# Kernel tuning notes

Hardware: AMD Instinct MI355X
Metric: run time of the kernel (lower is better)

Reference implementation:

```python
import jax, jax.numpy as jnp
import numpy as np

FP8_MAX = 448.0  # e4m3fn max representable magnitude


def _fp8_round(t):
    # round-trip through float8_e4m3fn emulates fp8 quantization rounding
    return t.astype(jnp.float8_e4m3fn).astype(t.dtype)


def setup_inputs() -> dict:
    key = jax.random.key(0)
    kx, kw, kb, ks = jax.random.split(key, 4)
    B, S, IN, OUT = 4, 2048, 4096, 4096
    x = jax.random.normal(kx, (B, S, IN), dtype=jnp.float16)
    # build an fp8-quantized weight exactly as the torch module does
    w = jax.random.uniform(kw, (OUT, IN), dtype=jnp.float16)
    w_s = (jnp.max(jnp.abs(w)).astype(jnp.float32) / FP8_MAX).reshape(1)
    w_fp8 = ((w.astype(jnp.float32) / w_s)
             .astype(jnp.float8_e4m3fn)
             .astype(jnp.float16))
    bias = jax.random.uniform(kb, (OUT,), dtype=jnp.float16)
    input_scale = jnp.ones((1,), dtype=jnp.float32)
    return {"x": x, "weight_fp8": w_fp8, "bias": bias,
            "input_scale": input_scale, "weight_scale": w_s}


def reference(x, weight_fp8, bias, input_scale, weight_scale):
    in_s = input_scale[0]
    w_s = weight_scale[0]
    # fake-quantize input to fp8 (per-tensor scale, clamp to e4m3 range)
    xq = jnp.clip(x.astype(jnp.float32) / in_s, -FP8_MAX, FP8_MAX)
    x_dq = _fp8_round(xq) * in_s                      # [B,S,IN] f32
    # dequantize fp8 weight
    w_dq = weight_fp8.astype(jnp.float32) * w_s       # [OUT,IN] f32
    out = jnp.einsum('bsi,oi->bso', x_dq, w_dq) + bias.astype(jnp.float32)
    return out.astype(x.dtype)
```

## Files before the change

### kernel.cpp

```cpp
#include <hip/hip_runtime.h>
#include <stdint.h>

typedef float  f32x4  __attribute__((ext_vector_type(4)));
typedef float  float4v __attribute__((ext_vector_type(4)));
typedef int    i32x4  __attribute__((ext_vector_type(4)));
typedef int    i32x8  __attribute__((ext_vector_type(8)));
typedef unsigned int u32x4 __attribute__((ext_vector_type(4)));

#define BM 128
#define BN 256
#define BKB 128

__device__ __forceinline__ unsigned f32_to_e4m3_sw(float t) {
    unsigned u = __float_as_uint(t);
    unsigned s = (u >> 24) & 0x80u;
    float ax = fabsf(t);
    if (ax < 0.015625f) {
        int m = (int)rintf(ax * 512.0f);
        return s | (unsigned)m;
    }
    unsigned au = u & 0x7fffffffu;
    unsigned r = au + 0x7FFFFu + ((au >> 20) & 1u);
    return s | (((r >> 23) - 120u) << 3) | ((r >> 20) & 7u);
}

__device__ __forceinline__ unsigned pack4_e4m3(float a, float b, float c, float d) {
#if __has_builtin(__builtin_amdgcn_cvt_pk_fp8_f32)
    int v = 0;
    v = __builtin_amdgcn_cvt_pk_fp8_f32(a, b, v, false);
    v = __builtin_amdgcn_cvt_pk_fp8_f32(c, d, v, true);
    return (unsigned)v;
#else
    return f32_to_e4m3_sw(a) | (f32_to_e4m3_sw(b) << 8) |
           (f32_to_e4m3_sw(c) << 16) | (f32_to_e4m3_sw(d) << 24);
#endif
}

__global__ void quant_kernel(const float4v* __restrict__ x, u32x4* __restrict__ xout, long nx16,
                             const float4v* __restrict__ w, u32x4* __restrict__ wout, long nw16,
                             const float* __restrict__ in_scale) {
    const float inv = 1.0f / in_scale[0];
    const long stride = (long)gridDim.x * blockDim.x;
    long i0 = (long)blockIdx.x * blockDim.x + threadIdx.x;
    for (long i = i0; i < nx16; i += stride) {
        u32x4 q;
#pragma unroll
        for (int j = 0; j < 4; ++j) {
            float4v v = x[i * 4 + j];
            float t0 = fminf(fmaxf(v[0] * inv, -448.0f), 448.0f);
            float t1 = fminf(fmaxf(v[1] * inv, -448.0f), 448.0f);
            float t2 = fminf(fmaxf(v[2] * inv, -448.0f), 448.0f);
            float t3 = fminf(fmaxf(v[3] * inv, -448.0f), 448.0f);
            q[j] = pack4_e4m3(t0, t1, t2, t3);
        }
        xout[i] = q;
    }
    for (long i = i0; i < nw16; i += stride) {
        u32x4 q;
#pragma unroll
        for (int j = 0; j < 4; ++j) {
            float4v v = w[i * 4 + j];
            q[j] = pack4_e4m3(v[0], v[1], v[2], v[3]);
        }
        wout[i] = q;
    }
}


__global__ __launch_bounds__(256, 2) void gemm_kernel(
    const unsigned char* __restrict__ A,
    const unsigned char* __restrict__ W,
    const float* __restrict__ bias,
    const float* __restrict__ in_scale,
    const float* __restrict__ w_scale,
    float* __restrict__ C, int M, int N, int K)
{
    __shared__ __align__(16) unsigned char sA[BM * BKB];
    __shared__ __align__(16) unsigned char sB[BN * BKB];

    const int tid  = threadIdx.x;
    const int wave = tid >> 6;
    const int lane = tid & 63;
    const int wr   = wave >> 1;
    const int wc   = wave & 1;

    const int nwg = gridDim.x;
    int bid = blockIdx.x, wgid;
    if ((nwg & 7) == 0) { const int cpx = nwg >> 3; wgid = (bid & 7) * cpx + (bid >> 3); }
    else wgid = bid;

    const int ntn = N / BN;
    int brow, bcol;
    if (nwg % (8 * ntn) == 0) {
        const int chunkId = wgid / (8 * ntn);
        const int local   = wgid % (8 * ntn);
        brow = (chunkId * 8 + (local & 7)) * BM;
        bcol = (local >> 3) * BN;
    } else {
        brow = (wgid / ntn) * BM;
        bcol = (wgid % ntn) * BN;
    }

    const int rowInChunk = lane >> 3;
    const int pPhys      = (lane & 7) ^ rowInChunk;
    const int slotSrc    = 2 * (pPhys & 3) + (pPhys >> 2);

    f32x4 acc[4][8];
#pragma unroll
    for (int i = 0; i < 4; ++i)
#pragma unroll
        for (int j = 0; j < 8; ++j) { f32x4 z = {0.f,0.f,0.f,0.f}; acc[i][j] = z; }

    const int g = lane >> 4;

    for (int kt = 0; kt < K; kt += BKB) {
        if (kt) __syncthreads();
#pragma unroll
        for (int c = 0; c < 4; ++c) {
            const int chunk = wave * 4 + c;
            const int row   = chunk * 8 + rowInChunk;
            const unsigned char* ga = A + (long)(brow + row) * K + kt + slotSrc * 16;
            __builtin_amdgcn_global_load_lds(
                (const __attribute__((address_space(1))) unsigned int*)ga,
                (__attribute__((address_space(3))) unsigned int*)(sA + chunk * 1024), 16, 0, 0);
        }
#pragma unroll
        for (int c = 0; c < 8; ++c) {
            const int chunk = wave * 8 + c;
            const int row   = chunk * 8 + rowInChunk;
            const unsigned char* gb = W + (long)(bcol + row) * K + kt + slotSrc * 16;
            __builtin_amdgcn_global_load_lds(
                (const __attribute__((address_space(1))) unsigned int*)gb,
                (__attribute__((address_space(3))) unsigned int*)(sB + chunk * 1024), 16, 0, 0);
        }
        __syncthreads();

        i32x8 af[4];
#pragma unroll
        for (int mi = 0; mi < 4; ++mi) {
            const int row = wr * 64 + mi * 16 + (lane & 15);
            const int sl  = g ^ (row & 7);
            i32x4 lo = *(const i32x4*)(sA + row * 128 + sl * 16);
            i32x4 hi = *(const i32x4*)(sA + row * 128 + (sl ^ 4) * 16);
            i32x8 t;
            t[0]=lo[0]; t[1]=lo[1]; t[2]=lo[2]; t[3]=lo[3];
            t[4]=hi[0]; t[5]=hi[1]; t[6]=hi[2]; t[7]=hi[3];
            af[mi] = t;
        }
#pragma unroll
        for (int ni = 0; ni < 8; ++ni) {
            const int row = wc * 128 + ni * 16 + (lane & 15);
            const int sl  = g ^ (row & 7);
            i32x4 lo = *(const i32x4*)(sB + row * 128 + sl * 16);
            i32x4 hi = *(const i32x4*)(sB + row * 128 + (sl ^ 4) * 16);
            i32x8 bf;
            bf[0]=lo[0]; bf[1]=lo[1]; bf[2]=lo[2]; bf[3]=lo[3];
            bf[4]=hi[0]; bf[5]=hi[1]; bf[6]=hi[2]; bf[7]=hi[3];
#pragma unroll
            for (int mi = 0; mi < 4; ++mi)
                acc[mi][ni] = __builtin_amdgcn_mfma_scale_f32_16x16x128_f8f6f4(
                    af[mi], bf, acc[mi][ni],
                    0, 0, 0, 0x7F7F7F7F, 0, 0x7F7F7F7F);
        }
    }

    const float sc = in_scale[0] * w_scale[0];
#pragma unroll
    for (int ni = 0; ni < 8; ++ni) {
        const int n   = bcol + wc * 128 + ni * 16 + (lane & 15);
        const float bv = bias[n];
#pragma unroll
        for (int mi = 0; mi < 4; ++mi) {
            const int m0 = brow + wr * 64 + mi * 16 + ((lane >> 4) << 2);
#pragma unroll
            for (int r = 0; r < 4; ++r)
                __builtin_nontemporal_store(fmaf(acc[mi][ni][r], sc, bv),
                                            &C[(long)(m0 + r) * N + n]);
        }
    }
}

extern "C" void kernel_launch(void* const* d_in, const int* in_sizes, int n_in,
                              void* d_out, int out_size, void* d_ws, size_t ws_size,
                              hipStream_t stream) {
    const float* x    = (const float*)d_in[0];
    const float* w    = (const float*)d_in[1];
    const float* bias = (const float*)d_in[2];
    const float* in_s = (const float*)d_in[3];
    const float* w_s  = (const float*)d_in[4];
    float* out = (float*)d_out;

    const int  N   = in_sizes[2];
    const long wsz = (long)in_sizes[1];
    const int  K   = (int)(wsz / N);
    const long xsz = (long)in_sizes[0];
    const int  M   = (int)(xsz / K);

    unsigned char* xq = (unsigned char*)d_ws;
    unsigned char* wq = xq + (size_t)M * K;

    quant_kernel<<<2048, 256, 0, stream>>>((const float4v*)x, (u32x4*)xq, xsz / 16,
                                           (const float4v*)w, (u32x4*)wq, wsz / 16, in_s);

    dim3 grid((M / BM) * (N / BN));
    gemm_kernel<<<grid, 256, 0, stream>>>(xq, wq, bias, in_s, w_s, out, M, N, K);
}
```

Baseline: 164.3 us.

## Switch GEMM to single-wave 64x128 tiles without workgroup barriers

Shrinks the GEMM block tile from 128x256 with four waves to 64x128 with a single wave, so each workgroup's wave loads its whole tile and replaces __syncthreads with explicit s_waitcnt on vmcnt/lgkmcnt. The block-to-tile mapping is reworked to group blocks along rows within XCD chunks. The intent is to remove barrier overhead and raise occupancy, at the cost of less data reuse per block, more global/L2 traffic and no overlap between loads and MFMAs within a workgroup.

```diff
diff --git a/kernel.cpp b/kernel.cpp
--- a/kernel.cpp
+++ b/kernel.cpp
@@ -7,8 +7,8 @@
 typedef int    i32x8  __attribute__((ext_vector_type(8)));
 typedef unsigned int u32x4 __attribute__((ext_vector_type(4)));
 
-#define BM 128
-#define BN 256
+#define BM 64
+#define BN 128
 #define BKB 128
 
 __device__ __forceinline__ unsigned f32_to_e4m3_sw(float t) {
@@ -67,7 +67,7 @@
 }
 
 
-__global__ __launch_bounds__(256, 2) void gemm_kernel(
+__global__ __launch_bounds__(64, 2) void gemm_kernel(
     const unsigned char* __restrict__ A,
     const unsigned char* __restrict__ W,
     const float* __restrict__ bias,
@@ -78,24 +78,23 @@
     __shared__ __align__(16) unsigned char sA[BM * BKB];
     __shared__ __align__(16) unsigned char sB[BN * BKB];
 
-    const int tid  = threadIdx.x;
-    const int wave = tid >> 6;
-    const int lane = tid & 63;
-    const int wr   = wave >> 1;
-    const int wc   = wave & 1;
+    const int lane = threadIdx.x;
 
     const int nwg = gridDim.x;
     int bid = blockIdx.x, wgid;
     if ((nwg & 7) == 0) { const int cpx = nwg >> 3; wgid = (bid & 7) * cpx + (bid >> 3); }
     else wgid = bid;
 
-    const int ntn = N / BN;
+    const int nrows = M / BM;
+    const int ntn   = N / BN;
     int brow, bcol;
-    if (nwg % (8 * ntn) == 0) {
-        const int chunkId = wgid / (8 * ntn);
-        const int local   = wgid % (8 * ntn);
-        brow = (chunkId * 8 + (local & 7)) * BM;
-        bcol = (local >> 3) * BN;
+    if ((nwg & 7) == 0 && ((nwg >> 3) % nrows) == 0) {
+        const int cpx     = nwg >> 3;
+        const int chunkId = wgid / cpx;
+        const int local   = wgid % cpx;
+        const int cpc     = cpx / nrows;
+        brow = (local % nrows) * BM;
+        bcol = (chunkId * cpc + local / nrows) * BN;
     } else {
         brow = (wgid / ntn) * BM;
         bcol = (wgid % ntn) * BN;
@@ -114,31 +113,31 @@
     const int g = lane >> 4;
 
     for (int kt = 0; kt < K; kt += BKB) {
-        if (kt) __syncthreads();
-#pragma unroll
-        for (int c = 0; c < 4; ++c) {
-            const int chunk = wave * 4 + c;
-            const int row   = chunk * 8 + rowInChunk;
+        if (kt) asm volatile("s_waitcnt lgkmcnt(0)" ::: "memory");
+
+#pragma unroll
+        for (int c = 0; c < 8; ++c) {
+            const int row = c * 8 + rowInChunk;
             const unsigned char* ga = A + (long)(brow + row) * K + kt + slotSrc * 16;
             __builtin_amdgcn_global_load_lds(
                 (const __attribute__((address_space(1))) unsigned int*)ga,
-                (__attribute__((address_space(3))) unsigned int*)(sA + chunk * 1024), 16, 0, 0);
-        }
-#pragma unroll
-        for (int c = 0; c < 8; ++c) {
-            const int chunk = wave * 8 + c;
-            const int row   = chunk * 8 + rowInChunk;
+                (__attribute__((address_space(3))) unsigned int*)(sA + c * 1024), 16, 0, 0);
+        }
+#pragma unroll
+        for (int c = 0; c < 16; ++c) {
+            const int row = c * 8 + rowInChunk;
             const unsigned char* gb = W + (long)(bcol + row) * K + kt + slotSrc * 16;
             __builtin_amdgcn_global_load_lds(
                 (const __attribute__((address_space(1))) unsigned int*)gb,
-                (__attribute__((address_space(3))) unsigned int*)(sB + chunk * 1024), 16, 0, 0);
-        }
-        __syncthreads();
+                (__attribute__((address_space(3))) unsigned int*)(sB + c * 1024), 16, 0, 0);
+        }
+        asm volatile("s_waitcnt vmcnt(0)" ::: "memory");
+        __builtin_amdgcn_sched_barrier(0);
 
         i32x8 af[4];
 #pragma unroll
         for (int mi = 0; mi < 4; ++mi) {
-            const int row = wr * 64 + mi * 16 + (lane & 15);
+            const int row = mi * 16 + (lane & 15);
             const int sl  = g ^ (row & 7);
             i32x4 lo = *(const i32x4*)(sA + row * 128 + sl * 16);
             i32x4 hi = *(const i32x4*)(sA + row * 128 + (sl ^ 4) * 16);
@@ -149,7 +148,7 @@
         }
 #pragma unroll
         for (int ni = 0; ni < 8; ++ni) {
-            const int row = wc * 128 + ni * 16 + (lane & 15);
+            const int row = ni * 16 + (lane & 15);
             const int sl  = g ^ (row & 7);
             i32x4 lo = *(const i32x4*)(sB + row * 128 + sl * 16);
             i32x4 hi = *(const i32x4*)(sB + row * 128 + (sl ^ 4) * 16);
@@ -167,11 +166,11 @@
     const float sc = in_scale[0] * w_scale[0];
 #pragma unroll
     for (int ni = 0; ni < 8; ++ni) {
-        const int n   = bcol + wc * 128 + ni * 16 + (lane & 15);
+        const int n   = bcol + ni * 16 + (lane & 15);
         const float bv = bias[n];
 #pragma unroll
         for (int mi = 0; mi < 4; ++mi) {
-            const int m0 = brow + wr * 64 + mi * 16 + ((lane >> 4) << 2);
+            const int m0 = brow + mi * 16 + ((lane >> 4) << 2);
 #pragma unroll
             for (int r = 0; r < 4; ++r)
                 __builtin_nontemporal_store(fmaf(acc[mi][ni][r], sc, bv),
@@ -203,5 +202,5 @@
                                            (const float4v*)w, (u32x4*)wq, wsz / 16, in_s);
 
     dim3 grid((M / BM) * (N / BN));
-    gemm_kernel<<<grid, 256, 0, stream>>>(xq, wq, bias, in_s, w_s, out, M, N, K);
-}
+    gemm_kernel<<<grid, 64, 0, stream>>>(xq, wq, bias, in_s, w_s, out, M, N, K);
+}
```

Result: slower. 216.3 us (+31.7%).
